# Optimization experiments

Measured on AMD Instinct MI355X. Metric: run time of the kernel, lower is better.

## Reference

```python
import jax, jax.numpy as jnp
import numpy as np

KERNEL_RATE = 0.5
AGG_DIS_RATE = 0.25
EPS = 1e-6
NUM_SEG = 9      # instance labels 0..8 (0 = background)
DELTA_AGG = 0.5  # PAN paper margin for aggregation loss
DELTA_DIS = 3.0  # PAN paper margin for discrimination loss


def setup_inputs() -> dict:
    key = jax.random.key(0)
    ks = jax.random.split(key, 6)
    B, H, W, C = 8, 640, 640, 4
    pre_text_logits = jax.random.normal(ks[0], (B, H, W), jnp.float32)
    pre_kernel_logits = jax.random.normal(ks[1], (B, H, W), jnp.float32)
    similarity_vector = jax.random.normal(ks[2], (B, C, H, W), jnp.float32)
    gt_text_key = jax.random.randint(ks[3], (B, H, W), 0, NUM_SEG).astype(jnp.int32)
    # kernels are shrunken text regions: subsample text-instance pixels
    gt_kernel_key = jnp.where(jax.random.uniform(ks[4], (B, H, W)) < 0.3,
                              gt_text_key, 0).astype(jnp.int32)
    gt_text = (gt_text_key > 0).astype(jnp.float32)
    gt_kernel = (gt_kernel_key > 0).astype(jnp.float32)
    train_mask = (jax.random.uniform(ks[5], (B, H, W)) > 0.05).astype(jnp.float32)
    return dict(pre_text_logits=pre_text_logits,
                pre_kernel_logits=pre_kernel_logits,
                similarity_vector=similarity_vector,
                gt_text=gt_text, gt_kernel=gt_kernel, train_mask=train_mask,
                gt_text_key=gt_text_key, gt_kernel_key=gt_kernel_key)


def dice_loss(pred, gt, mask, eps=EPS):
    B = pred.shape[0]
    p = (pred * mask).reshape(B, -1)
    g = (gt * mask).reshape(B, -1)
    a = jnp.sum(p * g, axis=1)
    b = jnp.sum(p * p, axis=1) + eps
    c = jnp.sum(g * g, axis=1) + eps
    return jnp.mean(1.0 - 2.0 * a / (b + c))


def ohem_single(score, gt, mask):
    n = score.size
    s = score.reshape(-1)
    g = gt.reshape(-1)
    m = mask.reshape(-1)
    pos = g > 0.5
    pos_num = jnp.sum(pos & (m > 0.5))
    neg = ~pos
    k = jnp.minimum(3 * pos_num, jnp.sum(neg))
    neg_scores = jnp.where(neg, s, -jnp.inf)
    sorted_desc = -jnp.sort(-neg_scores)          # descending
    thr = sorted_desc[jnp.clip(k - 1, 0, n - 1)]
    sel = ((s >= thr) | pos) & (m > 0.5)
    fallback = m > 0.5
    out = jnp.where((pos_num == 0) | (k == 0), fallback, sel)
    return out.astype(jnp.float32).reshape(score.shape)


ohem_batch = jax.vmap(ohem_single)


def agg_dis_single(F, lt, lk):
    # F: [C,H,W] embedding; lt/lk: [H,W] int instance labels (0=bg)
    C = F.shape[0]
    Ff = F.reshape(C, -1).T                        # [HW, C]
    lt = lt.reshape(-1)
    lk = lk.reshape(-1)
    ones = jnp.ones(lt.shape, jnp.float32)
    cnt_k = jax.ops.segment_sum(ones, lk, num_segments=NUM_SEG)   # [S]
    sum_k = jax.ops.segment_sum(Ff, lk, num_segments=NUM_SEG)    # [S,C]
    K = sum_k / jnp.maximum(cnt_k, 1.0)[:, None]   # kernel mean embeddings
    # aggregation: pull text pixels toward their instance's kernel mean
    d = jnp.linalg.norm(Ff - K[lt], axis=-1)       # [HW]
    pl = jnp.log(jnp.maximum(d - DELTA_AGG, 0.0) ** 2 + 1.0)
    cnt_t = jax.ops.segment_sum(ones, lt, num_segments=NUM_SEG)
    sum_l = jax.ops.segment_sum(pl, lt, num_segments=NUM_SEG)
    inst = sum_l / jnp.maximum(cnt_t, 1.0)
    idx = jnp.arange(NUM_SEG)
    valid = (cnt_t > 0) & (cnt_k > 0) & (idx > 0)
    nv = jnp.maximum(jnp.sum(valid), 1).astype(jnp.float32)
    L_agg = jnp.sum(jnp.where(valid, inst, 0.0)) / nv
    # discrimination: push kernel means of distinct instances apart
    vk = (cnt_k > 0) & (idx > 0)
    Kd = jnp.linalg.norm(K[:, None, :] - K[None, :, :], axis=-1)  # [S,S]
    dl = jnp.log(jnp.maximum(DELTA_DIS - Kd, 0.0) ** 2 + 1.0)
    pv = vk[:, None] & vk[None, :] & (idx[:, None] != idx[None, :])
    npair = jnp.maximum(jnp.sum(pv), 1).astype(jnp.float32)
    L_dis = jnp.sum(jnp.where(pv, dl, 0.0)) / npair
    return L_agg, L_dis


def reference(pre_text_logits, pre_kernel_logits, similarity_vector,
              gt_text, gt_kernel, train_mask, gt_text_key, gt_kernel_key):
    pre_text = jax.nn.sigmoid(pre_text_logits)
    pre_kernel = jax.nn.sigmoid(pre_kernel_logits)
    sel_t = pre_text > 0.5
    sel_k = pre_kernel > 0.5
    tm = train_mask > 0.5
    # predicted-positive masking of instance label maps
    lt = jnp.where(sel_t & tm, gt_text_key, 0)
    lk = jnp.where(sel_k & tm, gt_kernel_key, 0)
    # kernel dice loss, mask detached (numpy round-trip in original)
    km = jax.lax.stop_gradient((sel_t & tm).astype(jnp.float32))
    loss_kernel = dice_loss(pre_kernel, gt_kernel, km)
    # text dice loss with OHEM-selected mask (detached in original)
    om = jax.lax.stop_gradient(ohem_batch(pre_text, gt_text, train_mask))
    loss_text = dice_loss(pre_text, gt_text, om)
    La, Ld = jax.vmap(agg_dis_single)(similarity_vector, lt, lk)
    loss_agg = jnp.mean(La)
    loss_dis = jnp.mean(Ld)
    loss = loss_text + KERNEL_RATE * loss_kernel + AGG_DIS_RATE * (loss_agg + loss_dis)
    return loss
```

## Files before the change

kernel.cpp:

```cpp
#include <hip/hip_runtime.h>
#include <math.h>

#define BATCH 8
#define HW_N 409600
#define HW4 (HW_N / 4)
#define NBLK 200

#define NP 56
#define J_AK   0
#define J_BK   1
#define J_CK   2
#define J_AT   3
#define J_BTP  4
#define J_BTN  5
#define J_CNTK 6
#define J_CNTT 14
#define J_SUMK 22
#define J_CPOS 54
#define J_CNEG 55

__device__ __forceinline__ unsigned f2key(float x) {
    unsigned u = __float_as_uint(x);
    return (u & 0x80000000u) ? ~u : (u | 0x80000000u);
}
__device__ __forceinline__ float key2f(unsigned k) {
    unsigned u = (k & 0x80000000u) ? (k & 0x7fffffffu) : ~k;
    return __uint_as_float(u);
}
__device__ __forceinline__ float wred64(float v) {
#pragma unroll
    for (int o = 32; o > 0; o >>= 1) v += __shfl_xor(v, o, 64);
    return v;
}
__device__ __forceinline__ float wredmin64(float v) {
#pragma unroll
    for (int o = 32; o > 0; o >>= 1) v = fminf(v, __shfl_xor(v, o, 64));
    return v;
}
__device__ __forceinline__ float f4c(const float4& v, int p) {
    return p == 0 ? v.x : p == 1 ? v.y : p == 2 ? v.z : v.w;
}
__device__ __forceinline__ int i4c(const int4& v, int p) {
    return p == 0 ? v.x : p == 1 ? v.y : p == 2 ? v.z : v.w;
}

__global__ __launch_bounds__(256)
void k1_main(const float4* __restrict__ Tl, const float4* __restrict__ Kl,
             const float4* __restrict__ Fv, const float4* __restrict__ Tm,
             const int4* __restrict__ Ltk, const int4* __restrict__ Lkk,
             float* __restrict__ part, unsigned* __restrict__ pk8,
             unsigned* __restrict__ minkeyinv) {
    const int b = blockIdx.y;
    const int tid = threadIdx.x;
    const long base4 = (long)b * HW4;
    const long f04 = (long)b * 4 * HW4;

    __shared__ float sK[32];
    __shared__ unsigned cK[8], cT[8];
    __shared__ float bacc[6];
    __shared__ float wmin[4];
    __shared__ unsigned cP[4], cN[4];
    if (tid < 32) sK[tid] = 0.f;
    if (tid >= 32 && tid < 40) cK[tid - 32] = 0u;
    if (tid >= 40 && tid < 48) cT[tid - 40] = 0u;
    if (tid >= 48 && tid < 54) bacc[tid - 48] = 0.f;
    __syncthreads();

    float r0 = 0.f, r1 = 0.f, r2 = 0.f, r3 = 0.f, r4 = 0.f, r5 = 0.f;
    float vmin = INFINITY;
    unsigned cpos = 0, cneg = 0;

#pragma unroll
    for (int it = 0; it < 2; ++it) {
        const int i4 = blockIdx.x * 512 + it * 256 + tid;
        const float4 tl4 = Tl[base4 + i4];
        const float4 kl4 = Kl[base4 + i4];
        const float4 tm4 = Tm[base4 + i4];
        const int4 lt4 = Ltk[base4 + i4];
        const int4 lk4 = Lkk[base4 + i4];
        const float4 F0v = Fv[f04 + i4];
        const float4 F1v = Fv[f04 + HW4 + i4];
        const float4 F2v = Fv[f04 + 2 * HW4 + i4];
        const float4 F3v = Fv[f04 + 3 * HW4 + i4];
        unsigned pkw = 0;
#pragma unroll
        for (int p = 0; p < 4; ++p) {
            float tl = f4c(tl4, p), kl = f4c(kl4, p), m = f4c(tm4, p);
            int ltk = i4c(lt4, p), lkk = i4c(lk4, p);
            bool tm = m > 0.5f;
            bool selt = tl > 0.f;
            bool selk = kl > 0.f;
            bool pos = ltk > 0;
            float gkf = (lkk > 0) ? 1.f : 0.f;
            float km = (selt && tm) ? 1.f : 0.f;
            float pkv = 1.f / (1.f + __expf(-kl));
            float ptv = 1.f / (1.f + __expf(-tl));
            r0 = fmaf(pkv * gkf, km, r0);
            r1 = fmaf(pkv * pkv, km, r1);
            r2 = fmaf(gkf, km, r2);
            float ptm = (pos && tm) ? 1.f : 0.f;
            float ntm = (!pos && tm) ? 1.f : 0.f;
            r3 = fmaf(ptv, ptm, r3);
            r4 = fmaf(ptv * ptv, ptm, r4);
            r5 = fmaf(ptv * ptv, ntm, r5);
            cpos += __popcll(__ballot(pos && tm));
            cneg += __popcll(__ballot(!pos));
            vmin = fminf(vmin, pos ? INFINITY : tl);
            int lt = (selt && tm) ? ltk : 0;
            int lk = (selk && tm) ? lkk : 0;
            if (lk > 0) {
                atomicAdd(&sK[(lk - 1) * 4 + 0], f4c(F0v, p));
                atomicAdd(&sK[(lk - 1) * 4 + 1], f4c(F1v, p));
                atomicAdd(&sK[(lk - 1) * 4 + 2], f4c(F2v, p));
                atomicAdd(&sK[(lk - 1) * 4 + 3], f4c(F3v, p));
                atomicAdd(&cK[lk - 1], 1u);
            }
            if (lt > 0) atomicAdd(&cT[lt - 1], 1u);
            unsigned byte = (tm ? 1u : 0u) | (selt ? 2u : 0u) | ((unsigned)ltk << 2);
            pkw |= byte << (8 * p);
        }
        pk8[base4 + i4] = pkw;
    }

    r0 = wred64(r0); r1 = wred64(r1); r2 = wred64(r2);
    r3 = wred64(r3); r4 = wred64(r4); r5 = wred64(r5);
    vmin = wredmin64(vmin);
    const int wid = tid >> 6, lane = tid & 63;
    if (lane == 0) {
        atomicAdd(&bacc[0], r0); atomicAdd(&bacc[1], r1); atomicAdd(&bacc[2], r2);
        atomicAdd(&bacc[3], r3); atomicAdd(&bacc[4], r4); atomicAdd(&bacc[5], r5);
        wmin[wid] = vmin; cP[wid] = cpos; cN[wid] = cneg;
    }
    __syncthreads();

    float v = 0.f; bool w = true;
    if (tid < 6) v = bacc[tid];
    else if (tid < 14) v = (float)cK[tid - 6];
    else if (tid < 22) v = (float)cT[tid - 14];
    else if (tid < 54) v = sK[tid - 22];
    else if (tid == 54) v = (float)(cP[0] + cP[1] + cP[2] + cP[3]);
    else if (tid == 55) v = (float)(cN[0] + cN[1] + cN[2] + cN[3]);
    else w = false;
    if (w) part[((size_t)b * NP + tid) * NBLK + blockIdx.x] = v;
    if (tid == 56) {
        float mn = fminf(fminf(wmin[0], wmin[1]), fminf(wmin[2], wmin[3]));
        if (mn < INFINITY) atomicMax(&minkeyinv[b], ~f2key(mn));
    }
}

__global__ __launch_bounds__(256)
void k1_reduce(const float* __restrict__ part, const unsigned* __restrict__ minkeyinv,
               float* __restrict__ k1s, float* __restrict__ kms,
               float* __restrict__ thr, unsigned* __restrict__ kval,
               unsigned* __restrict__ fb) {
    const int b = blockIdx.x;
    const int tid = threadIdx.x, wid = tid >> 6, lane = tid & 63;
    __shared__ float ss[NP];
    __shared__ unsigned sfb;
    for (int j = wid; j < NP; j += 4) {
        const float* p = part + ((size_t)b * NP + j) * NBLK;
        float v = 0.f;
        for (int i = lane; i < NBLK; i += 64) v += p[i];
        v = wred64(v);
        if (lane == 0) ss[j] = v;
    }
    __syncthreads();
    if (tid == 0) {
        unsigned pos = (unsigned)(ss[J_CPOS] + 0.5f);
        unsigned neg = (unsigned)(ss[J_CNEG] + 0.5f);
        unsigned k = min(3u * pos, neg);
        kval[b] = k;
        unsigned f;
        if (pos == 0u || k == 0u) { thr[b] = -INFINITY; f = 1u; }
        else if (k == neg)        { thr[b] = key2f(~minkeyinv[b]); f = 1u; }
        else                      { f = 0u; }
        fb[b] = f; sfb = f;
    }
    __syncthreads();
    if (tid < NP)
        k1s[b * NP + tid] = (tid == J_BTN && sfb == 0u) ? 0.f : ss[tid];
    if (tid >= 64 && tid < 96) {
        int t = tid - 64, s = t >> 2;
        kms[b * 32 + t] = ss[J_SUMK + t] / fmaxf(ss[J_CNTK + s], 1.f);
    }
}

__global__ __launch_bounds__(256)
void k_rare(const float* __restrict__ Tl, const unsigned char* __restrict__ pk8,
            const unsigned* __restrict__ fb, const unsigned* __restrict__ kval,
            float* __restrict__ thr) {
    const int b = blockIdx.x;
    if (fb[b]) return;
    __shared__ unsigned hist[256];
    __shared__ unsigned sj, spre;
    const long base = (long)b * HW_N;
    if (threadIdx.x == 0) { sj = kval[b]; spre = 0u; }
    __syncthreads();
    for (int pass = 0; pass < 4; ++pass) {
        const int shift = 24 - 8 * pass;
        hist[threadIdx.x] = 0u;
        __syncthreads();
        const unsigned pref = spre;
        for (int i = threadIdx.x; i < HW_N; i += 256) {
            if (((pk8[base + i] >> 2) & 0xFu) != 0u) continue;
            unsigned key = f2key(Tl[base + i]);
            if (pass == 0 || (key >> (shift + 8)) == pref)
                atomicAdd(&hist[(key >> shift) & 0xFFu], 1u);
        }
        __syncthreads();
        if (threadIdx.x == 0) {
            unsigned j = sj, cum = 0;
            for (int d = 255; d >= 0; --d) {
                cum += hist[d];
                if (cum >= j) {
                    sj = j - (cum - hist[d]);
                    spre = (pref << 8) | (unsigned)d;
                    break;
                }
            }
        }
        __syncthreads();
    }
    if (threadIdx.x == 0) thr[b] = key2f(spre);
}

__global__ __launch_bounds__(256)
void k_negfix(const float4* __restrict__ Tl, const unsigned* __restrict__ pk8,
              const unsigned* __restrict__ fb, const float* __restrict__ thr,
              float* __restrict__ k1s) {
    const int b = blockIdx.y;
    if (fb[b]) return;
    const int tid = threadIdx.x;
    const long base4 = (long)b * HW4;
    const float tb = thr[b];
    float acc = 0.f;
#pragma unroll
    for (int it = 0; it < 2; ++it) {
        const int i4 = blockIdx.x * 512 + it * 256 + tid;
        const float4 tl4 = Tl[base4 + i4];
        const unsigned pkw = pk8[base4 + i4];
#pragma unroll
        for (int p = 0; p < 4; ++p) {
            unsigned byte = (pkw >> (8 * p)) & 0xFFu;
            bool tm = byte & 1u;
            bool neg = ((byte >> 2) & 0xFu) == 0u;
            float tl = f4c(tl4, p);
            if (neg && tm && tl >= tb) {
                float pt = 1.f / (1.f + __expf(-tl));
                acc = fmaf(pt, pt, acc);
            }
        }
    }
    acc = wred64(acc);
    __shared__ float wacc[4];
    if ((tid & 63) == 0) wacc[tid >> 6] = acc;
    __syncthreads();
    if (tid == 0)
        atomicAdd(&k1s[b * NP + J_BTN], wacc[0] + wacc[1] + wacc[2] + wacc[3]);
}

__global__ __launch_bounds__(256)
void k5_agg(const unsigned* __restrict__ pk8, const float4* __restrict__ Fv,
            const float* __restrict__ kms, float* __restrict__ sl) {
    const int b = blockIdx.y;
    const int tid = threadIdx.x;
    __shared__ float Kml[32];
    __shared__ float sL[8];
    if (tid < 32) Kml[tid] = kms[b * 32 + tid];
    if (tid >= 32 && tid < 40) sL[tid - 32] = 0.f;
    __syncthreads();
    const long base4 = (long)b * HW4;
    const long f04 = (long)b * 4 * HW4;
#pragma unroll
    for (int it = 0; it < 2; ++it) {
        const int i4 = blockIdx.x * 512 + it * 256 + tid;
        const unsigned pkw = pk8[base4 + i4];
        const float4 F0v = Fv[f04 + i4];
        const float4 F1v = Fv[f04 + HW4 + i4];
        const float4 F2v = Fv[f04 + 2 * HW4 + i4];
        const float4 F3v = Fv[f04 + 3 * HW4 + i4];
#pragma unroll
        for (int p = 0; p < 4; ++p) {
            unsigned byte = (pkw >> (8 * p)) & 0xFFu;
            int lt = ((byte & 3u) == 3u) ? (int)((byte >> 2) & 0xFu) : 0;
            if (lt > 0) {
                int kb = (lt - 1) * 4;
                float d0 = f4c(F0v, p) - Kml[kb + 0];
                float d1 = f4c(F1v, p) - Kml[kb + 1];
                float d2 = f4c(F2v, p) - Kml[kb + 2];
                float d3 = f4c(F3v, p) - Kml[kb + 3];
                float d = sqrtf(fmaf(d0, d0, fmaf(d1, d1, fmaf(d2, d2, d3 * d3))));
                float t = fmaxf(d - 0.5f, 0.f);
                atomicAdd(&sL[lt - 1], __logf(fmaf(t, t, 1.f)));
            }
        }
    }
    __syncthreads();
    if (tid < 8) atomicAdd(&sl[b * 8 + tid], sL[tid]);
}

__global__ __launch_bounds__(512)
void k6_final(const float* __restrict__ k1s, const float* __restrict__ kms,
              const float* __restrict__ sl, float* __restrict__ out) {
    const int tid = threadIdx.x;
    const int b = tid >> 6, lane = tid & 63;
    __shared__ float KmS[BATCH * 32];
    __shared__ float laS[BATCH], ldS[BATCH];
    if (tid < BATCH * 32) KmS[tid] = kms[tid];
    __syncthreads();
    const float* s1 = k1s + b * NP;

    float aggs = 0.f, aggc = 0.f;
    if (lane >= 1 && lane <= 8) {
        float ctv = s1[J_CNTT + lane - 1], ckv = s1[J_CNTK + lane - 1];
        if (ctv > 0.f && ckv > 0.f) {
            aggs = sl[b * 8 + lane - 1] / fmaxf(ctv, 1.f);
            aggc = 1.f;
        }
    }
    float diss = 0.f, disc = 0.f;
    {
        int i = 1 + (lane >> 3), j = 1 + (lane & 7);
        if (i != j && s1[J_CNTK + i - 1] > 0.f && s1[J_CNTK + j - 1] > 0.f) {
            float d2 = 0.f;
#pragma unroll
            for (int c = 0; c < 4; ++c) {
                float df = KmS[b * 32 + (i - 1) * 4 + c] - KmS[b * 32 + (j - 1) * 4 + c];
                d2 = fmaf(df, df, d2);
            }
            float kd = sqrtf(d2);
            float t = fmaxf(3.f - kd, 0.f);
            diss = logf(t * t + 1.f);
            disc = 1.f;
        }
    }
    aggs = wred64(aggs); aggc = wred64(aggc);
    diss = wred64(diss); disc = wred64(disc);
    if (lane == 0) {
        laS[b] = aggs / fmaxf(aggc, 1.f);
        ldS[b] = diss / fmaxf(disc, 1.f);
    }
    __syncthreads();
    if (tid == 0) {
        float Lt = 0.f, Lk = 0.f, La = 0.f, Ld = 0.f;
        for (int bb = 0; bb < BATCH; ++bb) {
            const float* a = k1s + bb * NP;
            Lk += 1.f - 2.f * a[J_AK] / ((a[J_BK] + 1e-6f) + (a[J_CK] + 1e-6f));
            float bt = a[J_BTP] + a[J_BTN];
            Lt += 1.f - 2.f * a[J_AT] / ((bt + 1e-6f) + (a[J_CPOS] + 1e-6f));
            La += laS[bb]; Ld += ldS[bb];
        }
        out[0] = Lt / BATCH + 0.5f * (Lk / BATCH) + 0.25f * (La / BATCH + Ld / BATCH);
    }
}

extern "C" void kernel_launch(void* const* d_in, const int* in_sizes, int n_in,
                              void* d_out, int out_size, void* d_ws, size_t ws_size,
                              hipStream_t stream) {
    (void)in_sizes; (void)n_in; (void)out_size; (void)ws_size;
    const float4* Tl = (const float4*)d_in[0];
    const float4* Kl = (const float4*)d_in[1];
    const float4* Fv = (const float4*)d_in[2];
    const float4* Tm = (const float4*)d_in[5];
    const int4* Ltk = (const int4*)d_in[6];
    const int4* Lkk = (const int4*)d_in[7];
    float* out = (float*)d_out;

    float* sl = (float*)d_ws;
    unsigned* minkeyinv = (unsigned*)(sl + 64);
    float* thr = (float*)(minkeyinv + 8);
    unsigned* kval = (unsigned*)(thr + 8);
    unsigned* fb = kval + 8;
    float* k1s = (float*)(fb + 8);
    float* kms = k1s + BATCH * NP;
    float* part = kms + BATCH * 32;
    unsigned* pk8 = (unsigned*)(part + (size_t)BATCH * NP * NBLK);

    hipMemsetAsync(d_ws, 0, (64 + 8) * 4, stream);

    dim3 g(NBLK, BATCH);
    k1_main<<<g, 256, 0, stream>>>(Tl, Kl, Fv, Tm, Ltk, Lkk, part, pk8, minkeyinv);
    k1_reduce<<<BATCH, 256, 0, stream>>>(part, minkeyinv, k1s, kms, thr, kval, fb);
    k_rare<<<BATCH, 256, 0, stream>>>((const float*)d_in[0],
                                      (const unsigned char*)pk8, fb, kval, thr);
    k_negfix<<<g, 256, 0, stream>>>(Tl, pk8, fb, thr, k1s);
    k5_agg<<<g, 256, 0, stream>>>(pk8, Fv, kms, sl);
    k6_final<<<1, 512, 0, stream>>>(k1s, kms, sl, out);
}
```

Measured before the change: 86.97 us.

## Fuse reduction and final kernels into last-block-done epilogues with global atomics

The per-block partial array and the separate k1_reduce kernel are replaced by global float atomics into k1s, plus a per-batch ticket counter. The last block of each batch computes the OHEM threshold decision and kernel means inline. The k6_final kernel is folded into k5_agg through a global ticket, and k5 now accumulates text counts and losses per label in registers using predicated FMAs instead of shared atomics. k_negfix now subtracts the below-threshold negatives instead of adding the above-threshold ones. This removes two launches and the partial-buffer round trip, at the cost of contended global atomics, threadfence overhead and non-deterministic float summation order.

```diff
diff --git a/kernel.cpp b/kernel.cpp
--- a/kernel.cpp
+++ b/kernel.cpp
@@ -6,18 +6,17 @@
 #define HW4 (HW_N / 4)
 #define NBLK 200
 
-#define NP 56
+#define NP 48
 #define J_AK   0
 #define J_BK   1
 #define J_CK   2
 #define J_AT   3
 #define J_BTP  4
 #define J_BTN  5
-#define J_CNTK 6
-#define J_CNTT 14
-#define J_SUMK 22
-#define J_CPOS 54
-#define J_CNEG 55
+#define J_CPOS 6
+#define J_CNEG 7
+#define J_CNTK 8
+#define J_SUMK 16
 
 __device__ __forceinline__ unsigned f2key(float x) {
     unsigned u = __float_as_uint(x);
@@ -48,22 +47,26 @@
 void k1_main(const float4* __restrict__ Tl, const float4* __restrict__ Kl,
              const float4* __restrict__ Fv, const float4* __restrict__ Tm,
              const int4* __restrict__ Ltk, const int4* __restrict__ Lkk,
-             float* __restrict__ part, unsigned* __restrict__ pk8,
-             unsigned* __restrict__ minkeyinv) {
+             float* __restrict__ k1s, unsigned* __restrict__ pk8,
+             unsigned* __restrict__ minkeyinv, unsigned* __restrict__ cnt1,
+             float* __restrict__ thr, unsigned* __restrict__ kval,
+             unsigned* __restrict__ fb, float* __restrict__ kms) {
     const int b = blockIdx.y;
     const int tid = threadIdx.x;
+    const int wid = tid >> 6, lane = tid & 63;
     const long base4 = (long)b * HW4;
     const long f04 = (long)b * 4 * HW4;
 
     __shared__ float sK[32];
-    __shared__ unsigned cK[8], cT[8];
-    __shared__ float bacc[6];
+    __shared__ unsigned cKs[8];
+    __shared__ float wacc[4][6];
     __shared__ float wmin[4];
-    __shared__ unsigned cP[4], cN[4];
+    __shared__ unsigned cPW[4], cNW[4];
+    __shared__ unsigned lastS;
+    __shared__ float ss[NP];
+
     if (tid < 32) sK[tid] = 0.f;
-    if (tid >= 32 && tid < 40) cK[tid - 32] = 0u;
-    if (tid >= 40 && tid < 48) cT[tid - 40] = 0u;
-    if (tid >= 48 && tid < 54) bacc[tid - 48] = 0.f;
+    else if (tid < 40) cKs[tid - 32] = 0u;
     __syncthreads();
 
     float r0 = 0.f, r1 = 0.f, r2 = 0.f, r3 = 0.f, r4 = 0.f, r5 = 0.f;
@@ -82,42 +85,39 @@
         const float4 F1v = Fv[f04 + HW4 + i4];
         const float4 F2v = Fv[f04 + 2 * HW4 + i4];
         const float4 F3v = Fv[f04 + 3 * HW4 + i4];
-        unsigned pkw = 0;
+        unsigned pkw = 0u;
 #pragma unroll
         for (int p = 0; p < 4; ++p) {
             float tl = f4c(tl4, p), kl = f4c(kl4, p), m = f4c(tm4, p);
             int ltk = i4c(lt4, p), lkk = i4c(lk4, p);
-            bool tm = m > 0.5f;
+            bool tmb = m > 0.5f;
             bool selt = tl > 0.f;
             bool selk = kl > 0.f;
             bool pos = ltk > 0;
             float gkf = (lkk > 0) ? 1.f : 0.f;
-            float km = (selt && tm) ? 1.f : 0.f;
+            float km = (selt && tmb) ? 1.f : 0.f;
             float pkv = 1.f / (1.f + __expf(-kl));
             float ptv = 1.f / (1.f + __expf(-tl));
             r0 = fmaf(pkv * gkf, km, r0);
             r1 = fmaf(pkv * pkv, km, r1);
             r2 = fmaf(gkf, km, r2);
-            float ptm = (pos && tm) ? 1.f : 0.f;
-            float ntm = (!pos && tm) ? 1.f : 0.f;
+            float ptm = (pos && tmb) ? 1.f : 0.f;
+            float ntm = (!pos && tmb) ? 1.f : 0.f;
             r3 = fmaf(ptv, ptm, r3);
             r4 = fmaf(ptv * ptv, ptm, r4);
             r5 = fmaf(ptv * ptv, ntm, r5);
-            cpos += __popcll(__ballot(pos && tm));
+            cpos += __popcll(__ballot(pos && tmb));
             cneg += __popcll(__ballot(!pos));
             vmin = fminf(vmin, pos ? INFINITY : tl);
-            int lt = (selt && tm) ? ltk : 0;
-            int lk = (selk && tm) ? lkk : 0;
+            int lk = (selk && tmb) ? lkk : 0;
             if (lk > 0) {
                 atomicAdd(&sK[(lk - 1) * 4 + 0], f4c(F0v, p));
                 atomicAdd(&sK[(lk - 1) * 4 + 1], f4c(F1v, p));
                 atomicAdd(&sK[(lk - 1) * 4 + 2], f4c(F2v, p));
                 atomicAdd(&sK[(lk - 1) * 4 + 3], f4c(F3v, p));
-                atomicAdd(&cK[lk - 1], 1u);
-            }
-            if (lt > 0) atomicAdd(&cT[lt - 1], 1u);
-            unsigned byte = (tm ? 1u : 0u) | (selt ? 2u : 0u) | ((unsigned)ltk << 2);
-            pkw |= byte << (8 * p);
+                atomicAdd(&cKs[lk - 1], 1u);
+            }
+            pkw |= ((tmb ? 1u : 0u) | (selt ? 2u : 0u) | ((unsigned)ltk << 2)) << (8 * p);
         }
         pk8[base4 + i4] = pkw;
     }
@@ -125,60 +125,43 @@
     r0 = wred64(r0); r1 = wred64(r1); r2 = wred64(r2);
     r3 = wred64(r3); r4 = wred64(r4); r5 = wred64(r5);
     vmin = wredmin64(vmin);
-    const int wid = tid >> 6, lane = tid & 63;
     if (lane == 0) {
-        atomicAdd(&bacc[0], r0); atomicAdd(&bacc[1], r1); atomicAdd(&bacc[2], r2);
-        atomicAdd(&bacc[3], r3); atomicAdd(&bacc[4], r4); atomicAdd(&bacc[5], r5);
-        wmin[wid] = vmin; cP[wid] = cpos; cN[wid] = cneg;
-    }
-    __syncthreads();
-
-    float v = 0.f; bool w = true;
-    if (tid < 6) v = bacc[tid];
-    else if (tid < 14) v = (float)cK[tid - 6];
-    else if (tid < 22) v = (float)cT[tid - 14];
-    else if (tid < 54) v = sK[tid - 22];
-    else if (tid == 54) v = (float)(cP[0] + cP[1] + cP[2] + cP[3]);
-    else if (tid == 55) v = (float)(cN[0] + cN[1] + cN[2] + cN[3]);
-    else w = false;
-    if (w) part[((size_t)b * NP + tid) * NBLK + blockIdx.x] = v;
-    if (tid == 56) {
+        wacc[wid][0] = r0; wacc[wid][1] = r1; wacc[wid][2] = r2;
+        wacc[wid][3] = r3; wacc[wid][4] = r4; wacc[wid][5] = r5;
+        wmin[wid] = vmin; cPW[wid] = cpos; cNW[wid] = cneg;
+    }
+    __syncthreads();
+    float v = 0.f;
+    if (tid < 6) v = wacc[0][tid] + wacc[1][tid] + wacc[2][tid] + wacc[3][tid];
+    else if (tid == 6) v = (float)(cPW[0] + cPW[1] + cPW[2] + cPW[3]);
+    else if (tid == 7) v = (float)(cNW[0] + cNW[1] + cNW[2] + cNW[3]);
+    else if (tid < 16) v = (float)cKs[tid - 8];
+    else if (tid < 48) v = sK[tid - 16];
+    if (tid < 48) atomicAdd(&k1s[b * NP + tid], v);
+    if (tid == 48) {
         float mn = fminf(fminf(wmin[0], wmin[1]), fminf(wmin[2], wmin[3]));
         if (mn < INFINITY) atomicMax(&minkeyinv[b], ~f2key(mn));
     }
-}
-
-__global__ __launch_bounds__(256)
-void k1_reduce(const float* __restrict__ part, const unsigned* __restrict__ minkeyinv,
-               float* __restrict__ k1s, float* __restrict__ kms,
-               float* __restrict__ thr, unsigned* __restrict__ kval,
-               unsigned* __restrict__ fb) {
-    const int b = blockIdx.x;
-    const int tid = threadIdx.x, wid = tid >> 6, lane = tid & 63;
-    __shared__ float ss[NP];
-    __shared__ unsigned sfb;
-    for (int j = wid; j < NP; j += 4) {
-        const float* p = part + ((size_t)b * NP + j) * NBLK;
-        float v = 0.f;
-        for (int i = lane; i < NBLK; i += 64) v += p[i];
-        v = wred64(v);
-        if (lane == 0) ss[j] = v;
-    }
+    __threadfence();
+    __syncthreads();
+    if (tid == 0) lastS = (atomicAdd(&cnt1[b], 1u) == NBLK - 1u) ? 1u : 0u;
+    __syncthreads();
+    if (!lastS) return;
+
+    __threadfence();
+    if (tid < NP) ss[tid] = atomicAdd(&k1s[b * NP + tid], 0.f);
     __syncthreads();
     if (tid == 0) {
         unsigned pos = (unsigned)(ss[J_CPOS] + 0.5f);
         unsigned neg = (unsigned)(ss[J_CNEG] + 0.5f);
         unsigned k = min(3u * pos, neg);
         kval[b] = k;
-        unsigned f;
-        if (pos == 0u || k == 0u) { thr[b] = -INFINITY; f = 1u; }
-        else if (k == neg)        { thr[b] = key2f(~minkeyinv[b]); f = 1u; }
-        else                      { f = 0u; }
-        fb[b] = f; sfb = f;
-    }
-    __syncthreads();
-    if (tid < NP)
-        k1s[b * NP + tid] = (tid == J_BTN && sfb == 0u) ? 0.f : ss[tid];
+        if (pos == 0u || k == 0u) { thr[b] = -INFINITY; fb[b] = 1u; }
+        else if (k == neg) {
+            unsigned cur = atomicMax(&minkeyinv[b], 0u);
+            thr[b] = key2f(~cur); fb[b] = 1u;
+        } else fb[b] = 0u;
+    }
     if (tid >= 64 && tid < 96) {
         int t = tid - 64, s = t >> 2;
         kms[b * 32 + t] = ss[J_SUMK + t] / fmaxf(ss[J_CNTK + s], 1.f);
@@ -186,7 +169,7 @@
 }
 
 __global__ __launch_bounds__(256)
-void k_rare(const float* __restrict__ Tl, const unsigned char* __restrict__ pk8,
+void k_rare(const float* __restrict__ Tl, const unsigned char* __restrict__ pk8b,
             const unsigned* __restrict__ fb, const unsigned* __restrict__ kval,
             float* __restrict__ thr) {
     const int b = blockIdx.x;
@@ -202,7 +185,7 @@
         __syncthreads();
         const unsigned pref = spre;
         for (int i = threadIdx.x; i < HW_N; i += 256) {
-            if (((pk8[base + i] >> 2) & 0xFu) != 0u) continue;
+            if ((pk8b[base + i] >> 2) != 0u) continue;
             unsigned key = f2key(Tl[base + i]);
             if (pass == 0 || (key >> (shift + 8)) == pref)
                 atomicAdd(&hist[(key >> shift) & 0xFFu], 1u);
@@ -242,35 +225,45 @@
 #pragma unroll
         for (int p = 0; p < 4; ++p) {
             unsigned byte = (pkw >> (8 * p)) & 0xFFu;
-            bool tm = byte & 1u;
-            bool neg = ((byte >> 2) & 0xFu) == 0u;
+            bool tmb = byte & 1u;
+            bool neg = (byte >> 2) == 0u;
             float tl = f4c(tl4, p);
-            if (neg && tm && tl >= tb) {
+            if (neg && tmb && tl < tb) {
                 float pt = 1.f / (1.f + __expf(-tl));
                 acc = fmaf(pt, pt, acc);
             }
         }
     }
     acc = wred64(acc);
-    __shared__ float wacc[4];
-    if ((tid & 63) == 0) wacc[tid >> 6] = acc;
-    __syncthreads();
-    if (tid == 0)
-        atomicAdd(&k1s[b * NP + J_BTN], wacc[0] + wacc[1] + wacc[2] + wacc[3]);
+    __shared__ float wa[4];
+    if ((tid & 63) == 0) wa[tid >> 6] = acc;
+    __syncthreads();
+    if (tid == 0) {
+        float s = wa[0] + wa[1] + wa[2] + wa[3];
+        if (s != 0.f) atomicAdd(&k1s[b * NP + J_BTN], -s);
+    }
 }
 
 __global__ __launch_bounds__(256)
 void k5_agg(const unsigned* __restrict__ pk8, const float4* __restrict__ Fv,
-            const float* __restrict__ kms, float* __restrict__ sl) {
+            const float* __restrict__ kms, const float* __restrict__ k1s,
+            float* __restrict__ slg, unsigned* __restrict__ tick,
+            float* __restrict__ out) {
     const int b = blockIdx.y;
-    const int tid = threadIdx.x;
+    const int tid = threadIdx.x, wid = tid >> 6, lane = tid & 63;
     __shared__ float Kml[32];
-    __shared__ float sL[8];
+    __shared__ float wacc[4][16];
+    __shared__ unsigned lastS;
+    __shared__ float laS[8], ldS[8];
+    __shared__ float KmS[256];
     if (tid < 32) Kml[tid] = kms[b * 32 + tid];
-    if (tid >= 32 && tid < 40) sL[tid - 32] = 0.f;
     __syncthreads();
     const long base4 = (long)b * HW4;
     const long f04 = (long)b * 4 * HW4;
+
+    float sl8[8] = {0.f, 0.f, 0.f, 0.f, 0.f, 0.f, 0.f, 0.f};
+    float ct8[8] = {0.f, 0.f, 0.f, 0.f, 0.f, 0.f, 0.f, 0.f};
+
 #pragma unroll
     for (int it = 0; it < 2; ++it) {
         const int i4 = blockIdx.x * 512 + it * 256 + tid;
@@ -282,63 +275,80 @@
 #pragma unroll
         for (int p = 0; p < 4; ++p) {
             unsigned byte = (pkw >> (8 * p)) & 0xFFu;
-            int lt = ((byte & 3u) == 3u) ? (int)((byte >> 2) & 0xFu) : 0;
-            if (lt > 0) {
-                int kb = (lt - 1) * 4;
-                float d0 = f4c(F0v, p) - Kml[kb + 0];
-                float d1 = f4c(F1v, p) - Kml[kb + 1];
-                float d2 = f4c(F2v, p) - Kml[kb + 2];
-                float d3 = f4c(F3v, p) - Kml[kb + 3];
-                float d = sqrtf(fmaf(d0, d0, fmaf(d1, d1, fmaf(d2, d2, d3 * d3))));
-                float t = fmaxf(d - 0.5f, 0.f);
-                atomicAdd(&sL[lt - 1], __logf(fmaf(t, t, 1.f)));
-            }
-        }
-    }
-    __syncthreads();
-    if (tid < 8) atomicAdd(&sl[b * 8 + tid], sL[tid]);
-}
-
-__global__ __launch_bounds__(512)
-void k6_final(const float* __restrict__ k1s, const float* __restrict__ kms,
-              const float* __restrict__ sl, float* __restrict__ out) {
-    const int tid = threadIdx.x;
-    const int b = tid >> 6, lane = tid & 63;
-    __shared__ float KmS[BATCH * 32];
-    __shared__ float laS[BATCH], ldS[BATCH];
-    if (tid < BATCH * 32) KmS[tid] = kms[tid];
-    __syncthreads();
-    const float* s1 = k1s + b * NP;
-
-    float aggs = 0.f, aggc = 0.f;
-    if (lane >= 1 && lane <= 8) {
-        float ctv = s1[J_CNTT + lane - 1], ckv = s1[J_CNTK + lane - 1];
-        if (ctv > 0.f && ckv > 0.f) {
-            aggs = sl[b * 8 + lane - 1] / fmaxf(ctv, 1.f);
-            aggc = 1.f;
-        }
-    }
-    float diss = 0.f, disc = 0.f;
-    {
-        int i = 1 + (lane >> 3), j = 1 + (lane & 7);
-        if (i != j && s1[J_CNTK + i - 1] > 0.f && s1[J_CNTK + j - 1] > 0.f) {
-            float d2 = 0.f;
-#pragma unroll
-            for (int c = 0; c < 4; ++c) {
-                float df = KmS[b * 32 + (i - 1) * 4 + c] - KmS[b * 32 + (j - 1) * 4 + c];
-                d2 = fmaf(df, df, d2);
-            }
-            float kd = sqrtf(d2);
-            float t = fmaxf(3.f - kd, 0.f);
-            diss = logf(t * t + 1.f);
-            disc = 1.f;
-        }
-    }
-    aggs = wred64(aggs); aggc = wred64(aggc);
-    diss = wred64(diss); disc = wred64(disc);
+            int lt = ((byte & 3u) == 3u) ? (int)(byte >> 2) : 0;
+            int kb = (lt > 0 ? lt - 1 : 0) * 4;
+            float d0 = f4c(F0v, p) - Kml[kb + 0];
+            float d1 = f4c(F1v, p) - Kml[kb + 1];
+            float d2 = f4c(F2v, p) - Kml[kb + 2];
+            float d3 = f4c(F3v, p) - Kml[kb + 3];
+            float d = sqrtf(fmaf(d0, d0, fmaf(d1, d1, fmaf(d2, d2, d3 * d3))));
+            float t = fmaxf(d - 0.5f, 0.f);
+            float pl = __logf(fmaf(t, t, 1.f));
+#pragma unroll
+            for (int s = 1; s <= 8; ++s) {
+                float e = (lt == s) ? 1.f : 0.f;
+                sl8[s - 1] = fmaf(e, pl, sl8[s - 1]);
+                ct8[s - 1] += e;
+            }
+        }
+    }
+
+#pragma unroll
+    for (int j = 0; j < 8; ++j) { sl8[j] = wred64(sl8[j]); ct8[j] = wred64(ct8[j]); }
     if (lane == 0) {
-        laS[b] = aggs / fmaxf(aggc, 1.f);
-        ldS[b] = diss / fmaxf(disc, 1.f);
+#pragma unroll
+        for (int j = 0; j < 8; ++j) { wacc[wid][j] = sl8[j]; wacc[wid][8 + j] = ct8[j]; }
+    }
+    __syncthreads();
+    if (tid < 16) {
+        float v = wacc[0][tid] + wacc[1][tid] + wacc[2][tid] + wacc[3][tid];
+        atomicAdd(&slg[b * 16 + tid], v);
+    }
+    __threadfence();
+    __syncthreads();
+    if (tid == 0) lastS = (atomicAdd(tick, 1u) == (unsigned)(NBLK * BATCH - 1)) ? 1u : 0u;
+    __syncthreads();
+    if (!lastS) return;
+
+    __threadfence();
+    KmS[tid] = kms[tid];
+    __syncthreads();
+#pragma unroll
+    for (int half = 0; half < 2; ++half) {
+        int bb = wid * 2 + half;
+        const float* s1 = k1s + bb * NP;
+        float aggs = 0.f, aggc = 0.f;
+        if (lane >= 1 && lane <= 8) {
+            float ctv = atomicAdd(&slg[bb * 16 + 8 + lane - 1], 0.f);
+            float ckv = s1[J_CNTK + lane - 1];
+            if (ctv > 0.f && ckv > 0.f) {
+                aggs = atomicAdd(&slg[bb * 16 + lane - 1], 0.f) / fmaxf(ctv, 1.f);
+                aggc = 1.f;
+            }
+        }
+        float diss = 0.f, disc = 0.f;
+        {
+            int i = 1 + (lane >> 3), j = 1 + (lane & 7);
+            if (i != j && s1[J_CNTK + i - 1] > 0.f && s1[J_CNTK + j - 1] > 0.f) {
+                float d2 = 0.f;
+#pragma unroll
+                for (int c = 0; c < 4; ++c) {
+                    float df = KmS[bb * 32 + (i - 1) * 4 + c] -
+                               KmS[bb * 32 + (j - 1) * 4 + c];
+                    d2 = fmaf(df, df, d2);
+                }
+                float kd = sqrtf(d2);
+                float t = fmaxf(3.f - kd, 0.f);
+                diss = __logf(fmaf(t, t, 1.f));
+                disc = 1.f;
+            }
+        }
+        aggs = wred64(aggs); aggc = wred64(aggc);
+        diss = wred64(diss); disc = wred64(disc);
+        if (lane == 0) {
+            laS[bb] = aggs / fmaxf(aggc, 1.f);
+            ldS[bb] = diss / fmaxf(disc, 1.f);
+        }
     }
     __syncthreads();
     if (tid == 0) {
@@ -346,8 +356,8 @@
         for (int bb = 0; bb < BATCH; ++bb) {
             const float* a = k1s + bb * NP;
             Lk += 1.f - 2.f * a[J_AK] / ((a[J_BK] + 1e-6f) + (a[J_CK] + 1e-6f));
-            float bt = a[J_BTP] + a[J_BTN];
-            Lt += 1.f - 2.f * a[J_AT] / ((bt + 1e-6f) + (a[J_CPOS] + 1e-6f));
+            float btv = a[J_BTP] + a[J_BTN];
+            Lt += 1.f - 2.f * a[J_AT] / ((btv + 1e-6f) + (a[J_CPOS] + 1e-6f));
             La += laS[bb]; Ld += ldS[bb];
         }
         out[0] = Lt / BATCH + 0.5f * (Lk / BATCH) + 0.25f * (La / BATCH + Ld / BATCH);
@@ -366,24 +376,26 @@
     const int4* Lkk = (const int4*)d_in[7];
     float* out = (float*)d_out;
 
-    float* sl = (float*)d_ws;
-    unsigned* minkeyinv = (unsigned*)(sl + 64);
-    float* thr = (float*)(minkeyinv + 8);
-    unsigned* kval = (unsigned*)(thr + 8);
-    unsigned* fb = kval + 8;
-    float* k1s = (float*)(fb + 8);
-    float* kms = k1s + BATCH * NP;
-    float* part = kms + BATCH * 32;
-    unsigned* pk8 = (unsigned*)(part + (size_t)BATCH * NP * NBLK);
-
-    hipMemsetAsync(d_ws, 0, (64 + 8) * 4, stream);
+    float* k1s = (float*)d_ws;
+    float* slg = k1s + BATCH * NP;
+    unsigned* minkeyinv = (unsigned*)(slg + BATCH * 16);
+    unsigned* cnt1 = minkeyinv + BATCH;
+    unsigned* tick = cnt1 + BATCH;
+    float* thr = (float*)(tick + 4);
+    unsigned* kval = (unsigned*)(thr + BATCH);
+    unsigned* fb = kval + BATCH;
+    float* kms = (float*)(fb + BATCH);
+    unsigned* pk8 = (unsigned*)(kms + BATCH * 32);
+
+    hipMemsetAsync(d_ws, 0,
+                   (size_t)(BATCH * NP + BATCH * 16 + BATCH + BATCH + 4) * 4,
+                   stream);
 
     dim3 g(NBLK, BATCH);
-    k1_main<<<g, 256, 0, stream>>>(Tl, Kl, Fv, Tm, Ltk, Lkk, part, pk8, minkeyinv);
-    k1_reduce<<<BATCH, 256, 0, stream>>>(part, minkeyinv, k1s, kms, thr, kval, fb);
+    k1_main<<<g, 256, 0, stream>>>(Tl, Kl, Fv, Tm, Ltk, Lkk, k1s, pk8,
+                                   minkeyinv, cnt1, thr, kval, fb, kms);
     k_rare<<<BATCH, 256, 0, stream>>>((const float*)d_in[0],
                                       (const unsigned char*)pk8, fb, kval, thr);
     k_negfix<<<g, 256, 0, stream>>>(Tl, pk8, fb, thr, k1s);
-    k5_agg<<<g, 256, 0, stream>>>(pk8, Fv, kms, sl);
-    k6_final<<<1, 512, 0, stream>>>(k1s, kms, sl, out);
-}
+    k5_agg<<<g, 256, 0, stream>>>(pk8, Fv, kms, k1s, slg, tick, out);
+}
```

Result: slower. 337.8 us (+288.4%).
